# Kernel optimization log

Measured on AMD Instinct MI355X. Metric: run time of the kernel, lower is better.

Reference implementation:

```python
import jax, jax.numpy as jnp
import numpy as np

B, S, D, H, R = 2, 2048, 1024, 16, 64
DD = D // H  # head depth = 64
EPS = 1e-06


def setup_inputs() -> dict:
    key = jax.random.key(0)
    ks = jax.random.split(key, 12)
    sc = 1.0 / np.sqrt(D)
    inp = {
        'v': jax.random.normal(ks[0], (B, S, D), jnp.float32),
        'k': jax.random.normal(ks[1], (B, S, D), jnp.float32),
        'q': jax.random.normal(ks[2], (B, S, D), jnp.float32),
        'wq_w': jax.random.normal(ks[3], (D, D), jnp.float32) * sc,
        'wq_b': jnp.zeros((D,), jnp.float32),
        'wk_w': jax.random.normal(ks[4], (D, D), jnp.float32) * sc,
        'wk_b': jnp.zeros((D,), jnp.float32),
        'wv_w': jax.random.normal(ks[5], (D, D), jnp.float32) * sc,
        'wv_b': jnp.zeros((D,), jnp.float32),
        'wc_w': jax.random.normal(ks[6], (D, D), jnp.float32) * sc,
        'wc_b': jnp.zeros((D,), jnp.float32),
        # random-feature projection (orthogonal in original; gaussian suffices for a math-equivalent reference)
        'wg': jax.random.normal(ks[7], (H, DD, R), jnp.float32) * (1.0 / np.sqrt(DD)),
    }
    return inp


def _split_heads(x):
    # [B,S,D] -> [B,H,S,DD]
    return x.reshape(B, S, H, DD).transpose(0, 2, 1, 3)


def _combine_heads(x):
    # [B,H,S,DD] -> [B,S,D]
    return x.transpose(0, 2, 1, 3).reshape(B, S, D)


def _sm_approx(x, wg):
    # x: [B,H,S,DD], wg: [H,DD,R] -> phi(x): [B,H,S,R]
    rsqr_d = 1.0 / np.sqrt(DD)
    h_x = jnp.exp(-0.5 * jnp.sum(jnp.square(x), axis=-1, keepdims=True))
    phi_x = rsqr_d * jnp.exp(jnp.einsum('bhsd,hdr->bhsr', x, wg))
    return h_x * phi_x


def reference(v, k, q, wq_w, wq_b, wk_w, wk_b, wv_w, wv_b, wc_w, wc_b, wg):
    norm_d = float(DD) ** -0.25
    qh = _split_heads((q @ wq_w + wq_b) * norm_d)   # [B,H,S,DD]
    kh = _split_heads((k @ wk_w + wk_b) * norm_d)   # [B,H,S,DD]
    vh = _split_heads(v @ wv_w + wv_b)              # [B,H,S,DD]

    q_prime = _sm_approx(qh, wg)                    # [B,H,S,R]
    k_prime = _sm_approx(kh, wg)                    # [B,H,S,R]

    # per-position outer product k_prime (x) v : [B,H,S,R,DD]
    kv_prime = jnp.einsum('bhsr,bhsd->bhsrd', k_prime, vh)

    # causal prefix sums over sequence axis (k_prev/kv_prev = 0 case)
    k_prefix = jnp.cumsum(k_prime, axis=2)          # [B,H,S,R]
    kv_prefix = jnp.cumsum(kv_prime, axis=2)        # [B,H,S,R,DD]

    qk_prefix = jnp.sum(q_prime * k_prefix, axis=-1, keepdims=True)       # [B,H,S,1]
    attn_unnorm = jnp.einsum('bhsr,bhsrd->bhsd', q_prime, kv_prefix)      # [B,H,S,DD]
    attn = attn_unnorm / (EPS + qk_prefix)

    out = _combine_heads(attn) @ wc_w + wc_b        # [B,S,D]
    return (k_prefix, kv_prefix, out)
```

## Files before the change

kernel.cpp:

```cpp
#include <hip/hip_runtime.h>
#include <hip/hip_bf16.h>

#define BB 2
#define SS 2048
#define DD 1024
#define HH 16
#define RR 64
#define DH 64
#define BH (BB*HH)
#define MM (BB*SS)
#define CH 32
#define NCH (SS/CH)
#define CSROW (RR*DH + RR)

using short8 = __attribute__((ext_vector_type(8))) short;
using f32x4  = __attribute__((ext_vector_type(4))) float;

typedef const __attribute__((address_space(1))) unsigned int* gp_t;
typedef __attribute__((address_space(3))) unsigned int* lp_t;

__device__ __forceinline__ void gll16(const void* g, void* l) {
    __builtin_amdgcn_global_load_lds((gp_t)g, (lp_t)l, 16, 0, 0);
}

__device__ __forceinline__ unsigned short f2bf(float x) {
    __hip_bfloat16 h = __float2bfloat16(x);
    return *(unsigned short*)&h;
}

__global__ __launch_bounds__(256) void k_pre(
    const float* __restrict__ q, const float* __restrict__ k, const float* __restrict__ v,
    const float* __restrict__ bq, const float* __restrict__ bk, const float* __restrict__ bv,
    const float* __restrict__ wq, const float* __restrict__ wk,
    const float* __restrict__ wv, const float* __restrict__ wc,
    const float* __restrict__ wg,
    __hip_bfloat16* __restrict__ Xb, float* __restrict__ biasb,
    __hip_bfloat16* __restrict__ WT, __hip_bfloat16* __restrict__ wcT,
    short* __restrict__ wgbT)
{
    int z = blockIdx.y;
    __shared__ float tile[64][65];
    if (z < 3) {
        const float* src = (z == 0) ? q : (z == 1) ? k : v;
        size_t i = ((size_t)blockIdx.x * 256 + threadIdx.x) * 4;
        float4 f = *(const float4*)(src + i);
        __hip_bfloat16* dst = Xb + (size_t)z * 4194304 + i;
        dst[0] = __float2bfloat16(f.x);
        dst[1] = __float2bfloat16(f.y);
        dst[2] = __float2bfloat16(f.z);
        dst[3] = __float2bfloat16(f.w);
        if (blockIdx.x == 0) {
            const float* bb = (z == 0) ? bq : (z == 1) ? bk : bv;
            for (int t = threadIdx.x; t < 1024; t += 256)
                biasb[z * 1024 + t] = bb[t];
        }
    } else if (z < 7) {
        if (blockIdx.x >= 256) return;
        int zz = z - 3;
        const float* W = (zz == 0) ? wq : (zz == 1) ? wk : (zz == 2) ? wv : wc;
        __hip_bfloat16* T = (zz < 3) ? (WT + (size_t)zz * 1048576) : wcT;
        int k0 = (blockIdx.x >> 4) * 64, n0 = (blockIdx.x & 15) * 64;
        for (int i = threadIdx.x; i < 4096; i += 256) {
            int r = i >> 6, cc = i & 63;
            tile[r][cc] = W[(size_t)(k0 + r) * 1024 + n0 + cc];
        }
        __syncthreads();
        for (int i = threadIdx.x; i < 4096; i += 256) {
            int nl = i >> 6, kl = i & 63;
            T[(size_t)(n0 + nl) * 1024 + k0 + kl] = __float2bfloat16(tile[kl][nl]);
        }
    } else {
        if (blockIdx.x >= 16) return;
        int hx = blockIdx.x;
        for (int i = threadIdx.x; i < 4096; i += 256)
            tile[i >> 6][i & 63] = wg[(size_t)hx * 4096 + i];
        __syncthreads();
        for (int i = threadIdx.x; i < 4096; i += 256) {
            int r = i >> 6, d = i & 63;
            wgbT[(size_t)hx * 4096 + r * 64 + d] = (short)f2bf(tile[d][r]);
        }
    }
}

__global__ __launch_bounds__(256) void gemm_bt(
    const __hip_bfloat16* __restrict__ X, const __hip_bfloat16* __restrict__ WT,
    const float* __restrict__ bias, float* __restrict__ Cout,
    const short* __restrict__ wgbT,
    float* __restrict__ qp_out, float* __restrict__ kp_out2,
    long zsX, long zsW, long zsB, long zsC, int mode)
{
    const int K = 1024, N = 1024;
    int z = blockIdx.z;
    const short* Xz = (const short*)(X + (size_t)z * zsX);
    const short* Wz = (const short*)(WT + (size_t)z * zsW);
    const float* bz = bias + (size_t)z * zsB;
    float* Cz = Cout + (size_t)z * zsC;

    __shared__ short smem[18432];
    short* As = smem;
    short* Bs = smem + 4096;
    short* wgT = smem;
    short* xw  = smem + 9216;

    int tid = threadIdx.x;
    int m0 = blockIdx.y * 128;
    int n0 = blockIdx.x * 128;
    int lane = tid & 63;
    int w = tid >> 6;
    int wm = (w >> 1) * 64, wn = (w & 1) * 64;

    f32x4 acc[4][4] = {};

    int srow = tid >> 2;
    int scol = (tid & 3) * 8;
    const short* Ag = Xz + (size_t)(m0 + srow) * K + scol;
    const short* Bg = Wz + (size_t)(n0 + srow) * K + scol;
    short* lA0 = As + tid * 8;
    short* lA1 = As + 64 * 32 + tid * 8;
    short* lB0 = Bs + tid * 8;
    short* lB1 = Bs + 64 * 32 + tid * 8;

    int fr = lane & 15, kg = (lane >> 4) * 8;

    for (int kt = 0; kt < K / 32; ++kt) {
        __syncthreads();
        gll16(Ag + kt * 32, lA0);
        gll16(Ag + (size_t)64 * K + kt * 32, lA1);
        gll16(Bg + kt * 32, lB0);
        gll16(Bg + (size_t)64 * K + kt * 32, lB1);
        __syncthreads();

        short8 af[4], bf[4];
#pragma unroll
        for (int mi = 0; mi < 4; ++mi)
            af[mi] = *(const short8*)&As[(wm + mi * 16 + fr) * 32 + kg];
#pragma unroll
        for (int ni = 0; ni < 4; ++ni)
            bf[ni] = *(const short8*)&Bs[(wn + ni * 16 + fr) * 32 + kg];
#pragma unroll
        for (int mi = 0; mi < 4; ++mi)
#pragma unroll
            for (int ni = 0; ni < 4; ++ni)
                acc[mi][ni] = __builtin_amdgcn_mfma_f32_16x16x32_bf16(af[mi], bf[ni], acc[mi][ni], 0, 0, 0);
    }

    int g = lane >> 4, c4 = lane & 15;

    if (mode == 1 && z < 2) {
        const float nd = 0.35355339059327373f;
        float* O = (z == 0) ? qp_out : kp_out2;
        int h = blockIdx.x * 2 + (w & 1);
        int b = m0 >> 11;
        float bias_n[4];
#pragma unroll
        for (int ni = 0; ni < 4; ++ni) bias_n[ni] = bz[n0 + wn + ni * 16 + c4];

        __syncthreads();
        {
            int row = tid >> 2, part = tid & 3;
#pragma unroll
            for (int hl = 0; hl < 2; ++hl) {
                const short* src = wgbT + ((size_t)(blockIdx.x * 2 + hl)) * 4096 + row * 64 + part * 16;
                short8 v0 = *(const short8*)src;
                short8 v1 = *(const short8*)(src + 8);
                *(short8*)&wgT[hl * 4608 + row * 72 + part * 16] = v0;
                *(short8*)&wgT[hl * 4608 + row * 72 + part * 16 + 8] = v1;
            }
        }
        __syncthreads();

        short* xww = xw + w * 2304;
        const short* wgh = wgT + (w & 1) * 4608;

#pragma unroll
        for (int pass = 0; pass < 2; ++pass) {
            float nrm[2][4];
#pragma unroll
            for (int mi_l = 0; mi_l < 2; ++mi_l) {
                int mi = pass * 2 + mi_l;
                float part_n[4] = {0.f, 0.f, 0.f, 0.f};
#pragma unroll
                for (int ni = 0; ni < 4; ++ni)
#pragma unroll
                    for (int i = 0; i < 4; ++i) {
                        float xv = (acc[mi][ni][i] + bias_n[ni]) * nd;
                        part_n[i] += xv * xv;
                        xww[(mi_l * 16 + g * 4 + i) * 72 + ni * 16 + c4] = (short)f2bf(xv);
                    }
#pragma unroll
                for (int i = 0; i < 4; ++i) {
                    float t = part_n[i];
                    t += __shfl_xor(t, 1, 64);
                    t += __shfl_xor(t, 2, 64);
                    t += __shfl_xor(t, 4, 64);
                    t += __shfl_xor(t, 8, 64);
                    nrm[mi_l][i] = t;
                }
            }
            short8 afr[2][2], bfr[4][2];
#pragma unroll
            for (int mi_l = 0; mi_l < 2; ++mi_l)
#pragma unroll
                for (int kk = 0; kk < 2; ++kk)
                    afr[mi_l][kk] = *(const short8*)&xww[(mi_l * 16 + c4) * 72 + kk * 32 + g * 8];
#pragma unroll
            for (int ri = 0; ri < 4; ++ri)
#pragma unroll
                for (int kk = 0; kk < 2; ++kk)
                    bfr[ri][kk] = *(const short8*)&wgh[(ri * 16 + c4) * 72 + kk * 32 + g * 8];
            f32x4 p[2][4] = {};
#pragma unroll
            for (int mi_l = 0; mi_l < 2; ++mi_l)
#pragma unroll
                for (int ri = 0; ri < 4; ++ri)
#pragma unroll
                    for (int kk = 0; kk < 2; ++kk)
                        p[mi_l][ri] = __builtin_amdgcn_mfma_f32_16x16x32_bf16(afr[mi_l][kk], bfr[ri][kk], p[mi_l][ri], 0, 0, 0);
#pragma unroll
            for (int mi_l = 0; mi_l < 2; ++mi_l)
#pragma unroll
                for (int ri = 0; ri < 4; ++ri)
#pragma unroll
                    for (int i = 0; i < 4; ++i) {
                        int mi = pass * 2 + mi_l;
                        float val = 0.125f * __expf(p[mi_l][ri][i] - 0.5f * nrm[mi_l][i]);
                        int row = m0 + wm + mi * 16 + g * 4 + i;
                        int s = row & 2047;
                        O[((size_t)(b * 16 + h) * SS + s) * RR + ri * 16 + c4] = val;
                    }
        }
        return;
    }

    int rg = g * 4;
#pragma unroll
    for (int mi = 0; mi < 4; ++mi)
#pragma unroll
        for (int ni = 0; ni < 4; ++ni) {
            int gn = n0 + wn + ni * 16 + fr;
            float bval = bz[gn];
#pragma unroll
            for (int i = 0; i < 4; ++i) {
                int gm = m0 + wm + mi * 16 + rg + i;
                Cz[(size_t)gm * N + gn] = acc[mi][ni][i] + bval;
            }
        }
}

__global__ __launch_bounds__(64) void k_chunksum(
    const float* __restrict__ kprime, const float* __restrict__ vh,
    float* __restrict__ cs)
{
    int c = blockIdx.x;
    int bh = blockIdx.y;
    int b = bh >> 4, h = bh & 15;
    int lane = threadIdx.x;
    __shared__ float kp[CH][RR];
    size_t rowbase = (size_t)bh * SS + c * CH;
    for (int i = 0; i < CH; ++i)
        kp[i][lane] = kprime[(rowbase + i) * RR + lane];
    __syncthreads();

    float st[RR];
#pragma unroll
    for (int r = 0; r < RR; ++r) st[r] = 0.f;
    float kpsum = 0.f;
    const float* vptr = vh + ((size_t)b * SS + c * CH) * DD + h * DH + lane;
    for (int s = 0; s < CH; ++s) {
        float vd = vptr[(size_t)s * DD];
        kpsum += kp[s][lane];
#pragma unroll
        for (int rq = 0; rq < RR / 4; ++rq) {
            float4 kq = *(const float4*)&kp[s][rq * 4];
            st[rq * 4 + 0] += kq.x * vd;
            st[rq * 4 + 1] += kq.y * vd;
            st[rq * 4 + 2] += kq.z * vd;
            st[rq * 4 + 3] += kq.w * vd;
        }
    }
    float* out = cs + (size_t)(bh * NCH + c) * CSROW;
#pragma unroll
    for (int r = 0; r < RR; ++r) out[r * 64 + lane] = st[r];
    out[4096 + lane] = kpsum;
}

__global__ __launch_bounds__(256) void k_scan(float* __restrict__ cs)
{
    int t = blockIdx.x * 256 + threadIdx.x;
    if (t >= BH * CSROW) return;
    int bh = t / CSROW;
    int e = t - bh * CSROW;
    float* p = cs + (size_t)bh * NCH * CSROW + e;
    float v[NCH];
#pragma unroll
    for (int c = 0; c < NCH; ++c) v[c] = p[(size_t)c * CSROW];
    float run = 0.f;
#pragma unroll
    for (int c = 0; c < NCH; ++c) {
        float x = v[c];
        p[(size_t)c * CSROW] = run;
        run += x;
    }
}

__global__ __launch_bounds__(64) void k_scanfinal(
    const float* __restrict__ kprime, const float* __restrict__ qprime,
    const float* __restrict__ vh, const float* __restrict__ cs,
    float* __restrict__ kp_out, float* __restrict__ kv_out,
    __hip_bfloat16* __restrict__ attnb)
{
    int c = blockIdx.x;
    int bh = blockIdx.y;
    int b = bh >> 4, h = bh & 15;
    int lane = threadIdx.x;
    int g = lane >> 4, c4 = lane & 15;
    __shared__ float kp[CH][RR];
    __shared__ float qp[CH][RR];
    size_t rowbase = (size_t)bh * SS + c * CH;
    for (int i = 0; i < CH; ++i) {
        kp[i][lane] = kprime[(rowbase + i) * RR + lane];
        qp[i][lane] = qprime[(rowbase + i) * RR + lane];
    }
    __syncthreads();

    const float* off = cs + (size_t)(bh * NCH + c) * CSROW;
    f32x4 st[16];
#pragma unroll
    for (int j = 0; j < 16; ++j)
        st[j] = *(const f32x4*)&off[(4 * j + g) * 64 + 4 * c4];
    float kps = off[4096 + lane];

    const float* vrow = vh + ((size_t)b * SS + c * CH) * DD + h * DH;
    for (int s = 0; s < CH; ++s) {
        float kpl = kp[s][lane];
        kps += kpl;
        size_t srow = rowbase + s;
        kp_out[srow * RR + lane] = kps;

        float qksum = qp[s][lane] * kps;
#pragma unroll
        for (int m = 1; m < 64; m <<= 1) qksum += __shfl_xor(qksum, m, 64);

        f32x4 v4 = *(const f32x4*)(vrow + (size_t)s * DD + 4 * c4);
        f32x4 accp = {0.f, 0.f, 0.f, 0.f};
        float* kvp = kv_out + srow * (size_t)(RR * DH);
#pragma unroll
        for (int j = 0; j < 16; ++j) {
            float kpj = kp[s][4 * j + g];
            float qpj = qp[s][4 * j + g];
            st[j] += kpj * v4;
            __builtin_nontemporal_store(st[j], (f32x4*)(kvp + (4 * j + g) * 64 + 4 * c4));
            accp += qpj * st[j];
        }
#pragma unroll
        for (int e = 0; e < 4; ++e) {
            accp[e] += __shfl_xor(accp[e], 16, 64);
            accp[e] += __shfl_xor(accp[e], 32, 64);
        }
        float rs = 1.0f / (1e-6f + qksum);
        if (g == 0) {
            ushort4 pkt;
            pkt.x = f2bf(accp[0] * rs);
            pkt.y = f2bf(accp[1] * rs);
            pkt.z = f2bf(accp[2] * rs);
            pkt.w = f2bf(accp[3] * rs);
            *(ushort4*)((unsigned short*)attnb + ((size_t)b * SS + c * CH + s) * DD + h * DH + 4 * c4) = pkt;
        }
    }
}

extern "C" void kernel_launch(void* const* d_in, const int* in_sizes, int n_in,
                              void* d_out, int out_size, void* d_ws, size_t ws_size,
                              hipStream_t stream) {
    const float* v_in  = (const float*)d_in[0];
    const float* k_in  = (const float*)d_in[1];
    const float* q_in  = (const float*)d_in[2];
    const float* wq_w  = (const float*)d_in[3];
    const float* wq_b  = (const float*)d_in[4];
    const float* wk_w  = (const float*)d_in[5];
    const float* wk_b  = (const float*)d_in[6];
    const float* wv_w  = (const float*)d_in[7];
    const float* wv_b  = (const float*)d_in[8];
    const float* wc_w  = (const float*)d_in[9];
    const float* wc_b  = (const float*)d_in[10];
    const float* wg    = (const float*)d_in[11];

    char* ws = (char*)d_ws;
    __hip_bfloat16* Xb    = (__hip_bfloat16*)(ws + 0);
    __hip_bfloat16* WT    = (__hip_bfloat16*)(ws + 25165824);
    __hip_bfloat16* wcT   = (__hip_bfloat16*)(ws + 31457280);
    float* biasb          = (float*)(ws + 33554432);
    float* qhkv           = (float*)(ws + 33570816);
    float* qprime         = (float*)(ws + 83902464);
    float* kprime         = (float*)(ws + 100679680);
    float* cs             = (float*)(ws + 117456896);
    __hip_bfloat16* attnb = (__hip_bfloat16*)(ws + 151535616);
    short* wgbT           = (short*)(ws + 159924224);

    float* kp_out = (float*)d_out;
    float* kv_out = kp_out + 4194304;
    float* out_o  = kv_out + 268435456;
    float* vh     = qhkv + 2 * 4194304;

    k_pre<<<dim3(4096, 8), 256, 0, stream>>>(q_in, k_in, v_in, wq_b, wk_b, wv_b,
                                             wq_w, wk_w, wv_w, wc_w, wg,
                                             Xb, biasb, WT, wcT, wgbT);
    gemm_bt<<<dim3(8, 32, 3), 256, 0, stream>>>(Xb, WT, biasb, qhkv, wgbT, qprime, kprime,
                                                4194304L, 1048576L, 1024L, 4194304L, 1);
    k_chunksum<<<dim3(NCH, BH), 64, 0, stream>>>(kprime, vh, cs);
    k_scan<<<dim3(520), 256, 0, stream>>>(cs);
    k_scanfinal<<<dim3(NCH, BH), 64, 0, stream>>>(kprime, qprime, vh, cs,
                                                  kp_out, kv_out, attnb);
    gemm_bt<<<dim3(8, 32, 1), 256, 0, stream>>>(attnb, wcT, wc_b, out_o, wgbT, qprime, kprime,
                                                0L, 0L, 0L, 0L, 0);
}
```

Measured before the change: 350.4 us.

## Compact prep grid, swizzle GEMM blocks, stage v tiles in LDS for scans

The prep kernel's 2D grid, where most blocks exited early, is replaced by a flat grid of only useful blocks. The GEMM gets an XCD-style block-index swizzle so neighbouring tiles share L2. The chunk-sum and final-scan kernels now load k', q' and v tiles with vectorized 16-byte loads into shared memory, replacing per-step strided global reads of v. This adds LDS usage per block and index arithmetic, and the swizzle assumes the block count is divisible by 8.

```diff
diff --git a/kernel.cpp b/kernel.cpp
--- a/kernel.cpp
+++ b/kernel.cpp
@@ -38,28 +38,31 @@
     __hip_bfloat16* __restrict__ WT, __hip_bfloat16* __restrict__ wcT,
     short* __restrict__ wgbT)
 {
-    int z = blockIdx.y;
+    int bid = blockIdx.x;
     __shared__ float tile[64][65];
-    if (z < 3) {
+    if (bid < 12288) {
+        int z = bid >> 12;
+        int bx = bid & 4095;
         const float* src = (z == 0) ? q : (z == 1) ? k : v;
-        size_t i = ((size_t)blockIdx.x * 256 + threadIdx.x) * 4;
+        size_t i = ((size_t)bx * 256 + threadIdx.x) * 4;
         float4 f = *(const float4*)(src + i);
         __hip_bfloat16* dst = Xb + (size_t)z * 4194304 + i;
         dst[0] = __float2bfloat16(f.x);
         dst[1] = __float2bfloat16(f.y);
         dst[2] = __float2bfloat16(f.z);
         dst[3] = __float2bfloat16(f.w);
-        if (blockIdx.x == 0) {
+        if (bx == 0) {
             const float* bb = (z == 0) ? bq : (z == 1) ? bk : bv;
             for (int t = threadIdx.x; t < 1024; t += 256)
                 biasb[z * 1024 + t] = bb[t];
         }
-    } else if (z < 7) {
-        if (blockIdx.x >= 256) return;
-        int zz = z - 3;
+    } else if (bid < 13312) {
+        int sub = bid - 12288;
+        int zz = sub >> 8;
+        sub &= 255;
         const float* W = (zz == 0) ? wq : (zz == 1) ? wk : (zz == 2) ? wv : wc;
         __hip_bfloat16* T = (zz < 3) ? (WT + (size_t)zz * 1048576) : wcT;
-        int k0 = (blockIdx.x >> 4) * 64, n0 = (blockIdx.x & 15) * 64;
+        int k0 = (sub >> 4) * 64, n0 = (sub & 15) * 64;
         for (int i = threadIdx.x; i < 4096; i += 256) {
             int r = i >> 6, cc = i & 63;
             tile[r][cc] = W[(size_t)(k0 + r) * 1024 + n0 + cc];
@@ -70,8 +73,7 @@
             T[(size_t)(n0 + nl) * 1024 + k0 + kl] = __float2bfloat16(tile[kl][nl]);
         }
     } else {
-        if (blockIdx.x >= 16) return;
-        int hx = blockIdx.x;
+        int hx = bid - 13312;
         for (int i = threadIdx.x; i < 4096; i += 256)
             tile[i >> 6][i & 63] = wg[(size_t)hx * 4096 + i];
         __syncthreads();
@@ -96,6 +98,15 @@
     const float* bz = bias + (size_t)z * zsB;
     float* Cz = Cout + (size_t)z * zsC;
 
+    int bid = blockIdx.y * gridDim.x + blockIdx.x;
+    int nb_cnt = gridDim.x * gridDim.y;
+    int cpx = nb_cnt >> 3;
+    int swz = (bid & 7) * cpx + (bid >> 3);
+    int nb = swz % gridDim.x;
+    int mb = swz / gridDim.x;
+    int m0 = mb * 128;
+    int n0 = nb * 128;
+
     __shared__ short smem[18432];
     short* As = smem;
     short* Bs = smem + 4096;
@@ -103,8 +114,6 @@
     short* xw  = smem + 9216;
 
     int tid = threadIdx.x;
-    int m0 = blockIdx.y * 128;
-    int n0 = blockIdx.x * 128;
     int lane = tid & 63;
     int w = tid >> 6;
     int wm = (w >> 1) * 64, wn = (w & 1) * 64;
@@ -149,7 +158,7 @@
     if (mode == 1 && z < 2) {
         const float nd = 0.35355339059327373f;
         float* O = (z == 0) ? qp_out : kp_out2;
-        int h = blockIdx.x * 2 + (w & 1);
+        int h = nb * 2 + (w & 1);
         int b = m0 >> 11;
         float bias_n[4];
 #pragma unroll
@@ -160,7 +169,7 @@
             int row = tid >> 2, part = tid & 3;
 #pragma unroll
             for (int hl = 0; hl < 2; ++hl) {
-                const short* src = wgbT + ((size_t)(blockIdx.x * 2 + hl)) * 4096 + row * 64 + part * 16;
+                const short* src = wgbT + ((size_t)(nb * 2 + hl)) * 4096 + row * 64 + part * 16;
                 short8 v0 = *(const short8*)src;
                 short8 v1 = *(const short8*)(src + 8);
                 *(short8*)&wgT[hl * 4608 + row * 72 + part * 16] = v0;
@@ -256,26 +265,32 @@
     int b = bh >> 4, h = bh & 15;
     int lane = threadIdx.x;
     __shared__ float kp[CH][RR];
+    __shared__ float vv[CH][RR];
     size_t rowbase = (size_t)bh * SS + c * CH;
-    for (int i = 0; i < CH; ++i)
-        kp[i][lane] = kprime[(rowbase + i) * RR + lane];
+    const float* vbase = vh + ((size_t)b * SS + c * CH) * DD + h * DH;
+#pragma unroll
+    for (int i = 0; i < 8; ++i) {
+        int flat = i * 64 + lane;
+        int row = flat >> 4, q4 = flat & 15;
+        *(f32x4*)&kp[row][q4 * 4] = *(const f32x4*)&kprime[(rowbase + row) * RR + q4 * 4];
+        *(f32x4*)&vv[row][q4 * 4] = *(const f32x4*)&vbase[(size_t)row * DD + q4 * 4];
+    }
     __syncthreads();
 
     float st[RR];
 #pragma unroll
     for (int r = 0; r < RR; ++r) st[r] = 0.f;
     float kpsum = 0.f;
-    const float* vptr = vh + ((size_t)b * SS + c * CH) * DD + h * DH + lane;
     for (int s = 0; s < CH; ++s) {
-        float vd = vptr[(size_t)s * DD];
+        float vd = vv[s][lane];
         kpsum += kp[s][lane];
 #pragma unroll
         for (int rq = 0; rq < RR / 4; ++rq) {
-            float4 kq = *(const float4*)&kp[s][rq * 4];
-            st[rq * 4 + 0] += kq.x * vd;
-            st[rq * 4 + 1] += kq.y * vd;
-            st[rq * 4 + 2] += kq.z * vd;
-            st[rq * 4 + 3] += kq.w * vd;
+            f32x4 kq = *(const f32x4*)&kp[s][rq * 4];
+            st[rq * 4 + 0] += kq[0] * vd;
+            st[rq * 4 + 1] += kq[1] * vd;
+            st[rq * 4 + 2] += kq[2] * vd;
+            st[rq * 4 + 3] += kq[3] * vd;
         }
     }
     float* out = cs + (size_t)(bh * NCH + c) * CSROW;
@@ -316,12 +331,17 @@
     int g = lane >> 4, c4 = lane & 15;
     __shared__ float kp[CH][RR];
     __shared__ float qp[CH][RR];
+    __shared__ float vv[CH][RR];
     size_t rowbase = (size_t)bh * SS + c * CH;
-    for (int i = 0; i < CH; ++i) {
-        kp[i][lane] = kprime[(rowbase + i) * RR + lane];
-        qp[i][lane] = qprime[(rowbase + i) * RR + lane];
-    }
-    __syncthreads();
+    const float* vbase = vh + ((size_t)b * SS + c * CH) * DD + h * DH;
+#pragma unroll
+    for (int i = 0; i < 8; ++i) {
+        int flat = i * 64 + lane;
+        int row = flat >> 4, q4 = flat & 15;
+        *(f32x4*)&kp[row][q4 * 4] = *(const f32x4*)&kprime[(rowbase + row) * RR + q4 * 4];
+        *(f32x4*)&qp[row][q4 * 4] = *(const f32x4*)&qprime[(rowbase + row) * RR + q4 * 4];
+        *(f32x4*)&vv[row][q4 * 4] = *(const f32x4*)&vbase[(size_t)row * DD + q4 * 4];
+    }
 
     const float* off = cs + (size_t)(bh * NCH + c) * CSROW;
     f32x4 st[16];
@@ -329,8 +349,8 @@
     for (int j = 0; j < 16; ++j)
         st[j] = *(const f32x4*)&off[(4 * j + g) * 64 + 4 * c4];
     float kps = off[4096 + lane];
-
-    const float* vrow = vh + ((size_t)b * SS + c * CH) * DD + h * DH;
+    __syncthreads();
+
     for (int s = 0; s < CH; ++s) {
         float kpl = kp[s][lane];
         kps += kpl;
@@ -341,7 +361,7 @@
 #pragma unroll
         for (int m = 1; m < 64; m <<= 1) qksum += __shfl_xor(qksum, m, 64);
 
-        f32x4 v4 = *(const f32x4*)(vrow + (size_t)s * DD + 4 * c4);
+        f32x4 v4 = *(const f32x4*)&vv[s][4 * c4];
         f32x4 accp = {0.f, 0.f, 0.f, 0.f};
         float* kvp = kv_out + srow * (size_t)(RR * DH);
 #pragma unroll
@@ -402,9 +422,9 @@
     float* out_o  = kv_out + 268435456;
     float* vh     = qhkv + 2 * 4194304;
 
-    k_pre<<<dim3(4096, 8), 256, 0, stream>>>(q_in, k_in, v_in, wq_b, wk_b, wv_b,
-                                             wq_w, wk_w, wv_w, wc_w, wg,
-                                             Xb, biasb, WT, wcT, wgbT);
+    k_pre<<<dim3(13328), 256, 0, stream>>>(q_in, k_in, v_in, wq_b, wk_b, wv_b,
+                                           wq_w, wk_w, wv_w, wc_w, wg,
+                                           Xb, biasb, WT, wcT, wgbT);
     gemm_bt<<<dim3(8, 32, 3), 256, 0, stream>>>(Xb, WT, biasb, qhkv, wgbT, qprime, kprime,
                                                 4194304L, 1048576L, 1024L, 4194304L, 1);
     k_chunksum<<<dim3(NCH, BH), 64, 0, stream>>>(kprime, vh, cs);
```

Result: faster. 342.4 us (-2.3%).
